# Kernel tuning notes

Hardware: AMD Instinct MI355X
Metric: run time of the kernel (lower is better)

## Reference

```python
import jax, jax.numpy as jnp
import numpy as np

NUM_HEADS = 4
D_MODEL = 256
HEAD_DIM = D_MODEL // NUM_HEADS  # 64
B, N = 4, 2048


def _pointwise_conv(w, b, x):
    # Conv1d(kernel_size=1): x [b, in, n] -> [b, out, n]
    return jnp.einsum('oi,bin->bon', w, x) + b[None, :, None]


def setup_inputs() -> dict:
    key = jax.random.key(0)
    ks = jax.random.split(key, 11)
    def g(k, shape, scale=1.0):
        return jax.random.normal(k, shape, dtype=jnp.float32) * scale
    return {
        'query': g(ks[0], (B, D_MODEL, N)),
        'key':   g(ks[1], (B, D_MODEL, N)),
        'value': g(ks[2], (B, D_MODEL, N)),
        'wq': g(ks[3], (D_MODEL, D_MODEL), 1.0 / np.sqrt(D_MODEL)),
        'bq': g(ks[4], (D_MODEL,), 0.02),
        'wk': g(ks[5], (D_MODEL, D_MODEL), 1.0 / np.sqrt(D_MODEL)),
        'bk': g(ks[6], (D_MODEL,), 0.02),
        'wv': g(ks[7], (D_MODEL, D_MODEL), 1.0 / np.sqrt(D_MODEL)),
        'bv': g(ks[8], (D_MODEL,), 0.02),
        'wm': g(ks[9], (D_MODEL, D_MODEL), 1.0 / np.sqrt(D_MODEL)),
        'bm': g(ks[10], (D_MODEL,), 0.02),
    }


def reference(query, key, value, wq, bq, wk, bk, wv, bv, wm, bm):
    b = query.shape[0]
    # Project and split heads: [b, d_model, n] -> [b, head_dim, heads, n]
    q = _pointwise_conv(wq, bq, query).reshape(b, HEAD_DIM, NUM_HEADS, -1)
    k = _pointwise_conv(wk, bk, key).reshape(b, HEAD_DIM, NUM_HEADS, -1)
    v = _pointwise_conv(wv, bv, value).reshape(b, HEAD_DIM, NUM_HEADS, -1)
    # scaled dot-product attention; scale is head dim (query.shape[1] in torch)
    scores = jnp.einsum('bdhn,bdhm->bhnm', q, k) / jnp.sqrt(jnp.float32(HEAD_DIM))
    prob = jax.nn.softmax(scores, axis=-1)
    x = jnp.einsum('bhnm,bdhm->bdhn', prob, v)
    # merge heads and final pointwise conv
    x = x.reshape(b, HEAD_DIM * NUM_HEADS, -1)
    return _pointwise_conv(wm, bm, x)
```

## Files before the change

### kernel.cpp

```cpp
#include <hip/hip_runtime.h>

typedef __attribute__((ext_vector_type(8))) short short8;
typedef __attribute__((ext_vector_type(4))) short short4v;
typedef __attribute__((ext_vector_type(4))) float f32x4;

#define MFMA_B16(a, b, c) __builtin_amdgcn_mfma_f32_16x16x32_bf16((a), (b), (c), 0, 0, 0)

#define NTOK 2048
#define DM 256
#define NB4 4
#define HD 64

__device__ __forceinline__ short f2bf(float f) {
  union { float f; unsigned u; } x;
  x.f = f;
  unsigned r = x.u + 0x7fffu + ((x.u >> 16) & 1u);
  return (short)(r >> 16);
}
__device__ __forceinline__ float bf2f(short s) {
  union { unsigned u; float f; } x;
  x.u = ((unsigned)(unsigned short)s) << 16;
  return x.f;
}

__device__ __forceinline__ void gload16(const short* g, short* l) {
  __builtin_amdgcn_global_load_lds(
      (const __attribute__((address_space(1))) void*)g,
      (__attribute__((address_space(3))) void*)l, 16, 0, 0);
}

__global__ __launch_bounds__(256) void k_wpre(const float* __restrict__ w0,
    const float* __restrict__ w1, const float* __restrict__ w2,
    const float* __restrict__ w3, short* __restrict__ wbf) {
  int t = blockIdx.x * 256 + threadIdx.x;
  const float* ws4[4] = {w0, w1, w2, w3};
  int base = t * 32;
#pragma unroll
  for (int blk = 0; blk < 4; blk++) {
    int off = base + blk * 8;
    int tau = off >> 16;
    int rest = off & 65535;
    int c = rest >> 8, ip = rest & 255;
    const float* srow = ws4[tau] + (size_t)c * 256;
    short8 r;
#pragma unroll
    for (int j = 0; j < 8; j++) {
      int i2 = ip + j;
      r[j] = (tau == 3) ? f2bf(srow[4 * (i2 & 63) + (i2 >> 6)]) : f2bf(srow[i2]);
    }
    *(short8*)(wbf + off) = r;
  }
}

__global__ __launch_bounds__(256, 4) void k_proj(const float* __restrict__ q,
    const float* __restrict__ k, const float* __restrict__ v,
    const short* __restrict__ wbf, const float* __restrict__ bq,
    const float* __restrict__ bk, const float* __restrict__ bv,
    short* __restrict__ qt, short* __restrict__ kt, short* __restrict__ vt) {
  __shared__ __align__(16) short As[16384];
  int z = blockIdx.y, b = z & 3, tau = z >> 2;
  const float* src = ((tau == 0) ? q : (tau == 1) ? k : v) + (size_t)b * DM * NTOK;
  const short* W = wbf + (size_t)tau * 65536;
  const float* bias = (tau == 0) ? bq : (tau == 1) ? bk : bv;
  int n0 = blockIdx.x * 64;
  int t = threadIdx.x;
  {
    int nseg = t & 15, rg = t >> 4;
#pragma unroll
    for (int outer = 0; outer < 2; outer++) {
      int iG = rg + 16 * outer;
      const float* s0 = src + (size_t)(iG * 8) * NTOK + n0 + nseg * 4;
      float4 rows[8];
#pragma unroll
      for (int j = 0; j < 8; j++) rows[j] = *(const float4*)(s0 + (size_t)j * NTOK);
      int i32 = iG >> 2, fhi = iG & 3, s = iG & 7;
#pragma unroll
      for (int e = 0; e < 4; e++) {
        int n = nseg * 4 + e;
        int nb = n >> 4, flo = n & 15;
        short8 r;
#pragma unroll
        for (int j = 0; j < 8; j++)
          r[j] = f2bf(e == 0 ? rows[j].x : e == 1 ? rows[j].y
                                         : e == 2 ? rows[j].z : rows[j].w);
        int frag = ((nb * 8 + i32) * 64 + fhi * 16 + flo) ^ s;
        *(short8*)(As + frag * 8) = r;
      }
    }
  }
  __syncthreads();
  int lane = t & 63, w = t >> 6;
  int lo = lane & 15, hi = lane >> 4;
  f32x4 acc[4][4] = {};
  const short* wrow = W + (size_t)(64 * w + lo) * DM + hi * 8;
#pragma unroll
  for (int ks = 0; ks < 8; ks++) {
    int sr = hi | ((ks & 1) << 2);
    short8 xf[4];
#pragma unroll
    for (int nb = 0; nb < 4; nb++) {
      int frag = ((nb * 8 + ks) * 64 + lane) ^ sr;
      xf[nb] = *(const short8*)(As + frag * 8);
    }
#pragma unroll
    for (int cb = 0; cb < 4; cb++) {
      short8 wf = *(const short8*)(wrow + (size_t)cb * 16 * DM + ks * 32);
      if (tau < 2) {
#pragma unroll
        for (int nb = 0; nb < 4; nb++)
          acc[cb][nb] = MFMA_B16(xf[nb], wf, acc[cb][nb]);
      } else {
#pragma unroll
        for (int nb = 0; nb < 4; nb++)
          acc[cb][nb] = MFMA_B16(wf, xf[nb], acc[cb][nb]);
      }
    }
  }
  if (tau < 2) {
    short* out = tau ? kt : qt;
    float scale = tau ? 1.0f : (0.125f * 1.44269504f);
#pragma unroll
    for (int cb = 0; cb < 4; cb++) {
      int c = 64 * w + 16 * cb + lo;
      float bvv = bias[c];
      int h = c & 3, d = c >> 2;
      int f = d >> 5, hif = (d >> 3) & 3, jj = d & 7;
#pragma unroll
      for (int nb = 0; nb < 4; nb++) {
        size_t n16 = (size_t)(b * 4 + h) * 128 + (n0 >> 4) + nb;
        short* ob = out + ((n16 * 2 + f) * 64 + hif * 16 + 4 * hi) * 8 + jj;
#pragma unroll
        for (int r = 0; r < 4; r++)
          ob[r * 8] = f2bf((acc[cb][nb][r] + bvv) * scale);
      }
    }
  } else {
#pragma unroll
    for (int cb = 0; cb < 4; cb++) {
#pragma unroll
      for (int r = 0; r < 4; r++) {
        int c = 64 * w + 16 * cb + 4 * hi + r;
        float bvv = bias[c];
        int h = c & 3, d = c >> 2;
        int db = d >> 4, rowd = d & 15;
        size_t bb64 = (size_t)(b * 4 + h) * 64;
#pragma unroll
        for (int nb = 0; nb < 4; nb++) {
          int n = n0 + 16 * nb + lo;
          int m32 = n >> 5, him = (n >> 3) & 3, jm = n & 7;
          vt[(((bb64 + m32) * 4 + db) * 64 + him * 16 + rowd) * 8 + jm] =
              f2bf(acc[cb][nb][r] + bvv);
        }
      }
    }
  }
}

template <int SPLIT>
__global__ __launch_bounds__(512, 4) void k_attn(const short* __restrict__ qt,
    const short* __restrict__ kt, const short* __restrict__ vt,
    short* __restrict__ opart, float* __restrict__ ml) {
  __shared__ __align__(16) short Ks[2][4096];
  __shared__ __align__(16) short Vs[2][4096];
  __shared__ __align__(16) short Ps[8][2][16][72];
  int z = blockIdx.z, b = z & 3, chunk = z >> 2;
  int h = blockIdx.y, n0 = blockIdx.x * 256;
  int lane = threadIdx.x & 63, w = threadIdx.x >> 6;
  int lo = lane & 15, hi = lane >> 4;
  const int CH = NTOK / SPLIT;
  const int kv0 = chunk * CH;
  int bh = b * 4 + h;
  const short* Qf = qt + (size_t)bh * 131072;
  const short* Kf = kt + (size_t)bh * 131072;
  const short* Vf = vt + (size_t)bh * 131072;
  short8 qf0[2], qf1[2];
#pragma unroll
  for (int qs = 0; qs < 2; qs++) {
    size_t n16 = (size_t)(n0 >> 4) + 8 * qs + w;
    qf0[qs] = *(const short8*)(Qf + ((n16 * 2 + 0) * 64 + lane) * 8);
    qf1[qs] = *(const short8*)(Qf + ((n16 * 2 + 1) * 64 + lane) * 8);
  }
  short8 ones;
#pragma unroll
  for (int j = 0; j < 8; j++) ones[j] = (short)0x3F80;
  f32x4 acc[2][4] = {};
  f32x4 accl[2] = {};

  int nt = CH >> 6, buf = 0;
  {
    const short* ksrc = Kf + (size_t)(kv0 >> 4) * 1024;
    const short* vsrc = Vf + (size_t)(kv0 >> 5) * 2048;
    gload16(ksrc + w * 512 + lane * 8, &Ks[0][w * 512]);
    gload16(vsrc + w * 512 + lane * 8, &Vs[0][w * 512]);
  }
  __syncthreads();

  for (int t = 0; t < nt; t++) {
    int m0 = kv0 + (t << 6);
    if (t + 1 < nt) {
      const short* ksrc = Kf + (size_t)((m0 + 64) >> 4) * 1024;
      const short* vsrc = Vf + (size_t)((m0 + 64) >> 5) * 2048;
      gload16(ksrc + w * 512 + lane * 8, &Ks[buf ^ 1][w * 512]);
      gload16(vsrc + w * 512 + lane * 8, &Vs[buf ^ 1][w * 512]);
    }
    f32x4 s[2][4];
    __builtin_amdgcn_s_setprio(1);
#pragma unroll
    for (int mb = 0; mb < 4; mb++) {
      short8 kf0 = *(const short8*)&Ks[buf][(mb * 2 + 0) * 512 + lane * 8];
      short8 kf1 = *(const short8*)&Ks[buf][(mb * 2 + 1) * 512 + lane * 8];
#pragma unroll
      for (int qs = 0; qs < 2; qs++) {
        f32x4 zz = {};
        zz = MFMA_B16(kf0, qf0[qs], zz);
        s[qs][mb] = MFMA_B16(kf1, qf1[qs], zz);
      }
    }
    __builtin_amdgcn_s_setprio(0);
#pragma unroll
    for (int qs = 0; qs < 2; qs++) {
#pragma unroll
      for (int mb = 0; mb < 4; mb++) {
        float e0 = exp2f(s[qs][mb][0]);
        float e1 = exp2f(s[qs][mb][1]);
        float e2 = exp2f(s[qs][mb][2]);
        float e3 = exp2f(s[qs][mb][3]);
        unsigned p01, p23;
        asm("v_cvt_pk_bf16_f32 %0, %1, %2" : "=v"(p01) : "v"(e0), "v"(e1));
        asm("v_cvt_pk_bf16_f32 %0, %1, %2" : "=v"(p23) : "v"(e2), "v"(e3));
        uint2 pk;
        pk.x = p01;
        pk.y = p23;
        *(uint2*)&Ps[w][qs][lo][16 * mb + 4 * hi] = pk;
      }
    }
    __builtin_amdgcn_s_setprio(1);
#pragma unroll
    for (int ks_i = 0; ks_i < 2; ks_i++) {
      short8 pa0 = *(const short8*)(&Ps[w][0][lo][32 * ks_i + 8 * hi]);
      short8 pa1 = *(const short8*)(&Ps[w][1][lo][32 * ks_i + 8 * hi]);
      accl[0] = MFMA_B16(pa0, ones, accl[0]);
      accl[1] = MFMA_B16(pa1, ones, accl[1]);
#pragma unroll
      for (int db = 0; db < 4; db++) {
        short8 vf = *(const short8*)&Vs[buf][(ks_i * 4 + db) * 512 + lane * 8];
        acc[0][db] = MFMA_B16(pa0, vf, acc[0][db]);
        acc[1][db] = MFMA_B16(pa1, vf, acc[1][db]);
      }
    }
    __builtin_amdgcn_s_setprio(0);
    __syncthreads();
    buf ^= 1;
  }

  size_t rbase = (((size_t)chunk * NB4 + b) * 4 + h) * NTOK;
#pragma unroll
  for (int qs = 0; qs < 2; qs++) {
    int nq = n0 + 128 * qs + 16 * w;
    if (lo == 0) {
#pragma unroll
      for (int r = 0; r < 4; r++)
        ml[rbase + nq + 4 * hi + r] = accl[qs][r];
    }
#pragma unroll
    for (int r = 0; r < 4; r++) {
      size_t row = rbase + nq + 4 * hi + r;
#pragma unroll
      for (int db = 0; db < 4; db++)
        opart[row * HD + 16 * db + lo] = f2bf(acc[qs][db][r]);
    }
  }
}

template <int NCH>
__global__ __launch_bounds__(256, 4) void k_out(const short* __restrict__ W,
    const short* __restrict__ opart, const float* __restrict__ ml,
    const float* __restrict__ bias, float* __restrict__ outp) {
  __shared__ __align__(16) short As[8192];
  int b = blockIdx.y;
  int n0 = blockIdx.x * 32;
  int t = threadIdx.x;
  int lane = t & 63, w = t >> 6;
  int lo16 = lane & 15, hi = lane >> 4;
  {
    int d8 = t & 7, h = (t >> 3) & 3, nb8 = t >> 5;
    int i32 = 2 * h + (d8 >> 2), fhi = d8 & 3;
#pragma unroll
    for (int it = 0; it < 4; it++) {
      int noff = nb8 * 4 + it;
      int n = n0 + noff;
      int nb = noff >> 4, flo = noff & 15;
      size_t row0 = ((size_t)b * 4 + h) * NTOK + n;
      float l = ml[row0];
      float o[8];
      short8 o0 = *(const short8*)(opart + row0 * HD + d8 * 8);
#pragma unroll
      for (int j = 0; j < 8; j++) o[j] = bf2f(o0[j]);
#pragma unroll
      for (int ch = 1; ch < NCH; ch++) {
        size_t rowc = row0 + (size_t)ch * 16 * NTOK;
        l += ml[rowc];
        short8 oc = *(const short8*)(opart + rowc * HD + d8 * 8);
#pragma unroll
        for (int j = 0; j < 8; j++) o[j] += bf2f(oc[j]);
      }
      float inv = 1.0f / l;
      short8 res;
#pragma unroll
      for (int j = 0; j < 8; j++) res[j] = f2bf(o[j] * inv);
      int frag = ((nb * 8 + i32) * 64 + fhi * 16 + flo) ^ d8;
      *(short8*)(As + frag * 8) = res;
    }
  }
  __syncthreads();
  f32x4 acc[4][2] = {};
  const short* arow = W + (size_t)(64 * w + lo16) * DM + hi * 8;
#pragma unroll
  for (int ks = 0; ks < 8; ks++) {
    int sr = hi | ((ks & 1) << 2);
    short8 bbr[2];
#pragma unroll
    for (int nb = 0; nb < 2; nb++) {
      int frag = ((nb * 8 + ks) * 64 + lane) ^ sr;
      bbr[nb] = *(const short8*)(As + frag * 8);
    }
#pragma unroll
    for (int cb = 0; cb < 4; cb++) {
      short8 a = *(const short8*)(arow + (size_t)cb * 16 * DM + ks * 32);
#pragma unroll
      for (int nb = 0; nb < 2; nb++)
        acc[cb][nb] = MFMA_B16(a, bbr[nb], acc[cb][nb]);
    }
  }
#pragma unroll
  for (int cb = 0; cb < 4; cb++) {
#pragma unroll
    for (int r = 0; r < 4; r++) {
      int c = 64 * w + 16 * cb + 4 * hi + r;
      float bvv = bias[c];
#pragma unroll
      for (int nb = 0; nb < 2; nb++) {
        int n = n0 + 16 * nb + lo16;
        outp[((size_t)b * DM + c) * NTOK + n] = acc[cb][nb][r] + bvv;
      }
    }
  }
}

extern "C" void kernel_launch(void* const* d_in, const int* in_sizes, int n_in,
                              void* d_out, int out_size, void* d_ws, size_t ws_size,
                              hipStream_t stream) {
  const float* q  = (const float*)d_in[0];
  const float* k  = (const float*)d_in[1];
  const float* v  = (const float*)d_in[2];
  const float* wq = (const float*)d_in[3];
  const float* bq = (const float*)d_in[4];
  const float* wk = (const float*)d_in[5];
  const float* bk = (const float*)d_in[6];
  const float* wv = (const float*)d_in[7];
  const float* bv = (const float*)d_in[8];
  const float* wm = (const float*)d_in[9];
  const float* bm = (const float*)d_in[10];

  char* ws = (char*)d_ws;
  const size_t MB = 1024 * 1024;
  short* Qt  = (short*)(ws);
  short* Kt  = (short*)(ws + 4 * MB);
  short* Vt  = (short*)(ws + 8 * MB);
  short* Wbf = (short*)(ws + 12 * MB);
  float* ML    = (float*)(ws + 13 * MB);
  short* Opart = (short*)(ws + 14 * MB);

  k_wpre<<<dim3(32), 256, 0, stream>>>(wq, wk, wv, wm, Wbf);
  k_proj<<<dim3(32, 12), 256, 0, stream>>>(q, k, v, Wbf, bq, bk, bv, Qt, Kt, Vt);

  if (ws_size >= 32 * MB) {
    k_attn<4><<<dim3(8, 4, 16), 512, 0, stream>>>(Qt, Kt, Vt, Opart, ML);
    k_out<4><<<dim3(64, 4), 256, 0, stream>>>(Wbf + 3 * 65536, Opart, ML, bm, (float*)d_out);
  } else {
    k_attn<1><<<dim3(8, 4, 4), 512, 0, stream>>>(Qt, Kt, Vt, Opart, ML);
    k_out<1><<<dim3(64, 4), 256, 0, stream>>>(Wbf + 3 * 65536, Opart, ML, bm, (float*)d_out);
  }

  (void)in_sizes; (void)n_in; (void)out_size; (void)ws_size;
}
```

Before: 69.81 us.

## Switch attention kernel to 32x32x16 MFMA with register-resident P via permlane swap

Rewrites the attention inner loop to use 32x32x16 bf16 MFMA instead of 16x16x32, with Q, K and V written by the projection kernel in new fragment-friendly layouts. The probability tile is repacked in registers with v_permlane32_swap, so the LDS round-trip for P is gone. Row sums are accumulated in VALU rather than through an MFMA against a ones vector. This cuts LDS traffic and MFMA instruction count per tile, but adds VALU adds and more accumulator registers, which may affect occupancy.

```diff
diff --git a/kernel.cpp b/kernel.cpp
--- a/kernel.cpp
+++ b/kernel.cpp
@@ -1,10 +1,11 @@
 #include <hip/hip_runtime.h>
 
 typedef __attribute__((ext_vector_type(8))) short short8;
-typedef __attribute__((ext_vector_type(4))) short short4v;
 typedef __attribute__((ext_vector_type(4))) float f32x4;
+typedef __attribute__((ext_vector_type(16))) float f32x16;
 
 #define MFMA_B16(a, b, c) __builtin_amdgcn_mfma_f32_16x16x32_bf16((a), (b), (c), 0, 0, 0)
+#define MFMA32(a, b, c) __builtin_amdgcn_mfma_f32_32x32x16_bf16((a), (b), (c), 0, 0, 0)
 
 #define NTOK 2048
 #define DM 256
@@ -124,15 +125,19 @@
       int c = 64 * w + 16 * cb + lo;
       float bvv = bias[c];
       int h = c & 3, d = c >> 2;
-      int f = d >> 5, hif = (d >> 3) & 3, jj = d & 7;
+      size_t base = (size_t)(b * 4 + h) * 64;
+      int dterm = (d & 31) + ((d >> 4) * 64) * 0;
 #pragma unroll
       for (int nb = 0; nb < 4; nb++) {
-        size_t n16 = (size_t)(b * 4 + h) * 128 + (n0 >> 4) + nb;
-        short* ob = out + ((n16 * 2 + f) * 64 + hif * 16 + 4 * hi) * 8 + jj;
-#pragma unroll
-        for (int r = 0; r < 4; r++)
-          ob[r * 8] = f2bf((acc[cb][nb][r] + bvv) * scale);
-      }
+#pragma unroll
+        for (int r = 0; r < 4; r++) {
+          int n = n0 + 16 * nb + 4 * hi + r;
+          size_t addr = (((base + (n >> 5)) * 4 + (d >> 4)) * 64 +
+                         (n & 31) + 32 * ((d >> 3) & 1)) * 8 + (d & 7);
+          out[addr] = f2bf((acc[cb][nb][r] + bvv) * scale);
+        }
+      }
+      (void)dterm;
     }
   } else {
 #pragma unroll
@@ -142,14 +147,13 @@
         int c = 64 * w + 16 * cb + 4 * hi + r;
         float bvv = bias[c];
         int h = c & 3, d = c >> 2;
-        int db = d >> 4, rowd = d & 15;
-        size_t bb64 = (size_t)(b * 4 + h) * 64;
+        size_t base = (size_t)(b * 4 + h) * 128;
 #pragma unroll
         for (int nb = 0; nb < 4; nb++) {
-          int n = n0 + 16 * nb + lo;
-          int m32 = n >> 5, him = (n >> 3) & 3, jm = n & 7;
-          vt[(((bb64 + m32) * 4 + db) * 64 + him * 16 + rowd) * 8 + jm] =
-              f2bf(acc[cb][nb][r] + bvv);
+          int m = n0 + 16 * nb + lo;
+          size_t addr = (((base + (m >> 4)) * 2 + (d >> 5)) * 64 +
+                         (d & 31) + 32 * ((m >> 3) & 1)) * 8 + (m & 7);
+          vt[addr] = f2bf(acc[cb][nb][r] + bvv);
         }
       }
     }
@@ -162,113 +166,83 @@
     short* __restrict__ opart, float* __restrict__ ml) {
   __shared__ __align__(16) short Ks[2][4096];
   __shared__ __align__(16) short Vs[2][4096];
-  __shared__ __align__(16) short Ps[8][2][16][72];
   int z = blockIdx.z, b = z & 3, chunk = z >> 2;
   int h = blockIdx.y, n0 = blockIdx.x * 256;
-  int lane = threadIdx.x & 63, w = threadIdx.x >> 6;
-  int lo = lane & 15, hi = lane >> 4;
+  int tid = threadIdx.x;
+  int lane = tid & 63, w = tid >> 6;
+  int l31 = lane & 31, hi2 = lane >> 5;
   const int CH = NTOK / SPLIT;
   const int kv0 = chunk * CH;
   int bh = b * 4 + h;
   const short* Qf = qt + (size_t)bh * 131072;
   const short* Kf = kt + (size_t)bh * 131072;
   const short* Vf = vt + (size_t)bh * 131072;
-  short8 qf0[2], qf1[2];
-#pragma unroll
-  for (int qs = 0; qs < 2; qs++) {
-    size_t n16 = (size_t)(n0 >> 4) + 8 * qs + w;
-    qf0[qs] = *(const short8*)(Qf + ((n16 * 2 + 0) * 64 + lane) * 8);
-    qf1[qs] = *(const short8*)(Qf + ((n16 * 2 + 1) * 64 + lane) * 8);
-  }
-  short8 ones;
-#pragma unroll
-  for (int j = 0; j < 8; j++) ones[j] = (short)0x3F80;
-  f32x4 acc[2][4] = {};
-  f32x4 accl[2] = {};
+  short8 qf[4];
+#pragma unroll
+  for (int dk = 0; dk < 4; dk++)
+    qf[dk] = *(const short8*)(Qf + (((size_t)((n0 >> 5) + w) * 4 + dk) * 64 + lane) * 8);
+  f32x16 acc[2] = {};
+  float lacc = 0.0f;
 
   int nt = CH >> 6, buf = 0;
-  {
-    const short* ksrc = Kf + (size_t)(kv0 >> 4) * 1024;
-    const short* vsrc = Vf + (size_t)(kv0 >> 5) * 2048;
-    gload16(ksrc + w * 512 + lane * 8, &Ks[0][w * 512]);
-    gload16(vsrc + w * 512 + lane * 8, &Vs[0][w * 512]);
-  }
+  gload16(Kf + (size_t)(kv0 >> 5) * 2048 + tid * 8, &Ks[0][tid * 8]);
+  gload16(Vf + (size_t)(kv0 >> 4) * 1024 + tid * 8, &Vs[0][tid * 8]);
   __syncthreads();
 
   for (int t = 0; t < nt; t++) {
     int m0 = kv0 + (t << 6);
     if (t + 1 < nt) {
-      const short* ksrc = Kf + (size_t)((m0 + 64) >> 4) * 1024;
-      const short* vsrc = Vf + (size_t)((m0 + 64) >> 5) * 2048;
-      gload16(ksrc + w * 512 + lane * 8, &Ks[buf ^ 1][w * 512]);
-      gload16(vsrc + w * 512 + lane * 8, &Vs[buf ^ 1][w * 512]);
-    }
-    f32x4 s[2][4];
-    __builtin_amdgcn_s_setprio(1);
-#pragma unroll
-    for (int mb = 0; mb < 4; mb++) {
-      short8 kf0 = *(const short8*)&Ks[buf][(mb * 2 + 0) * 512 + lane * 8];
-      short8 kf1 = *(const short8*)&Ks[buf][(mb * 2 + 1) * 512 + lane * 8];
-#pragma unroll
-      for (int qs = 0; qs < 2; qs++) {
-        f32x4 zz = {};
-        zz = MFMA_B16(kf0, qf0[qs], zz);
-        s[qs][mb] = MFMA_B16(kf1, qf1[qs], zz);
-      }
-    }
-    __builtin_amdgcn_s_setprio(0);
-#pragma unroll
-    for (int qs = 0; qs < 2; qs++) {
-#pragma unroll
-      for (int mb = 0; mb < 4; mb++) {
-        float e0 = exp2f(s[qs][mb][0]);
-        float e1 = exp2f(s[qs][mb][1]);
-        float e2 = exp2f(s[qs][mb][2]);
-        float e3 = exp2f(s[qs][mb][3]);
-        unsigned p01, p23;
-        asm("v_cvt_pk_bf16_f32 %0, %1, %2" : "=v"(p01) : "v"(e0), "v"(e1));
-        asm("v_cvt_pk_bf16_f32 %0, %1, %2" : "=v"(p23) : "v"(e2), "v"(e3));
-        uint2 pk;
-        pk.x = p01;
-        pk.y = p23;
-        *(uint2*)&Ps[w][qs][lo][16 * mb + 4 * hi] = pk;
-      }
-    }
-    __builtin_amdgcn_s_setprio(1);
-#pragma unroll
-    for (int ks_i = 0; ks_i < 2; ks_i++) {
-      short8 pa0 = *(const short8*)(&Ps[w][0][lo][32 * ks_i + 8 * hi]);
-      short8 pa1 = *(const short8*)(&Ps[w][1][lo][32 * ks_i + 8 * hi]);
-      accl[0] = MFMA_B16(pa0, ones, accl[0]);
-      accl[1] = MFMA_B16(pa1, ones, accl[1]);
-#pragma unroll
-      for (int db = 0; db < 4; db++) {
-        short8 vf = *(const short8*)&Vs[buf][(ks_i * 4 + db) * 512 + lane * 8];
-        acc[0][db] = MFMA_B16(pa0, vf, acc[0][db]);
-        acc[1][db] = MFMA_B16(pa1, vf, acc[1][db]);
-      }
-    }
-    __builtin_amdgcn_s_setprio(0);
+      gload16(Kf + (size_t)((m0 + 64) >> 5) * 2048 + tid * 8, &Ks[buf ^ 1][tid * 8]);
+      gload16(Vf + (size_t)((m0 + 64) >> 4) * 1024 + tid * 8, &Vs[buf ^ 1][tid * 8]);
+    }
+#pragma unroll
+    for (int mb2 = 0; mb2 < 2; mb2++) {
+      f32x16 s = {};
+      __builtin_amdgcn_s_setprio(1);
+#pragma unroll
+      for (int dk = 0; dk < 4; dk++) {
+        short8 kf = *(const short8*)&Ks[buf][(mb2 * 4 + dk) * 512 + lane * 8];
+        s = MFMA32(kf, qf[dk], s);
+      }
+      __builtin_amdgcn_s_setprio(0);
+#pragma unroll
+      for (int ks = 0; ks < 2; ks++) {
+        float e0 = exp2f(s[ks * 8 + 0]), e1 = exp2f(s[ks * 8 + 1]);
+        float e2 = exp2f(s[ks * 8 + 2]), e3 = exp2f(s[ks * 8 + 3]);
+        float e4 = exp2f(s[ks * 8 + 4]), e5 = exp2f(s[ks * 8 + 5]);
+        float e6 = exp2f(s[ks * 8 + 6]), e7 = exp2f(s[ks * 8 + 7]);
+        lacc += ((e0 + e1) + (e2 + e3)) + ((e4 + e5) + (e6 + e7));
+        unsigned A, B, C2, D2;
+        asm("v_cvt_pk_bf16_f32 %0, %1, %2" : "=v"(A) : "v"(e0), "v"(e1));
+        asm("v_cvt_pk_bf16_f32 %0, %1, %2" : "=v"(C2) : "v"(e2), "v"(e3));
+        asm("v_cvt_pk_bf16_f32 %0, %1, %2" : "=v"(B) : "v"(e4), "v"(e5));
+        asm("v_cvt_pk_bf16_f32 %0, %1, %2" : "=v"(D2) : "v"(e6), "v"(e7));
+        asm("v_permlane32_swap_b32 %0, %1" : "+v"(A), "+v"(B));
+        asm("v_permlane32_swap_b32 %0, %1" : "+v"(C2), "+v"(D2));
+        union { unsigned u[4]; short8 v8; } pu;
+        pu.u[0] = A; pu.u[1] = C2; pu.u[2] = B; pu.u[3] = D2;
+        __builtin_amdgcn_s_setprio(1);
+#pragma unroll
+        for (int dcol = 0; dcol < 2; dcol++) {
+          short8 vf = *(const short8*)&Vs[buf][((mb2 * 2 + ks) * 2 + dcol) * 512 + lane * 8];
+          acc[dcol] = MFMA32(pu.v8, vf, acc[dcol]);
+        }
+        __builtin_amdgcn_s_setprio(0);
+      }
+    }
     __syncthreads();
     buf ^= 1;
   }
 
+  float l = lacc + __shfl_xor(lacc, 32);
   size_t rbase = (((size_t)chunk * NB4 + b) * 4 + h) * NTOK;
-#pragma unroll
-  for (int qs = 0; qs < 2; qs++) {
-    int nq = n0 + 128 * qs + 16 * w;
-    if (lo == 0) {
-#pragma unroll
-      for (int r = 0; r < 4; r++)
-        ml[rbase + nq + 4 * hi + r] = accl[qs][r];
-    }
-#pragma unroll
-    for (int r = 0; r < 4; r++) {
-      size_t row = rbase + nq + 4 * hi + r;
-#pragma unroll
-      for (int db = 0; db < 4; db++)
-        opart[row * HD + 16 * db + lo] = f2bf(acc[qs][db][r]);
-    }
+  if (lane < 32) ml[rbase + n0 + 32 * w + lane] = l;
+#pragma unroll
+  for (int r = 0; r < 16; r++) {
+    int n = n0 + 32 * w + (r & 3) + 8 * (r >> 2) + 4 * hi2;
+#pragma unroll
+    for (int dcol = 0; dcol < 2; dcol++)
+      opart[(rbase + n) * HD + dcol * 32 + l31] = f2bf(acc[dcol][r]);
   }
 }
 
```

Result: no change. 69.44 us (-0.5%).
